# Performance work log

Measured on AMD Instinct MI355X. Metric: run time of the kernel, lower is better.

Reference implementation:

```python
import jax, jax.numpy as jnp
import numpy as np

N, D_IN, D, C, TOPK = 8192, 1024, 512, 2, 6
SCALE = D ** -0.5
LN_EPS = 1e-5


def setup_inputs() -> dict:
    key = jax.random.key(0)
    ks = jax.random.split(key, 20)
    s = 0.02
    p = {
        'x': jax.random.normal(ks[0], (N, D_IN), jnp.float32),
        'fc1_w': jax.random.normal(ks[1], (D_IN, D)) * s,
        'fc1_b': jnp.zeros((D,)),
        'wh_w': jax.random.normal(ks[2], (D, D)) * s,
        'wh_b': jnp.zeros((D,)),
        'wt_w': jax.random.normal(ks[3], (D, D)) * s,
        'wt_b': jnp.zeros((D,)),
        'lin1_w': jax.random.normal(ks[4], (D, D)) * s,
        'lin1_b': jnp.zeros((D,)),
        'lin2_w': jax.random.normal(ks[5], (D, D)) * s,
        'lin2_b': jnp.zeros((D,)),
        'att1_w': jax.random.normal(ks[6], (D, D // 2)) * s,
        'att1_b': jnp.zeros((D // 2,)),
        'att2_w': jax.random.normal(ks[7], (D // 2, 1)) * s,
        'att2_b': jnp.zeros((1,)),
        'ln_g': jnp.ones((D,)),
        'ln_b': jnp.zeros((D,)),
        'fc_w': jax.random.normal(ks[8], (D, C)) * s,
        'fc_b': jnp.zeros((C,)),
    }
    return p


def reference(x, fc1_w, fc1_b, wh_w, wh_b, wt_w, wt_b, lin1_w, lin1_b,
              lin2_w, lin2_b, att1_w, att1_b, att2_w, att2_b, ln_g, ln_b,
              fc_w, fc_b):
    # _fc1: Linear + ReLU (dropout = eval identity)
    h = jax.nn.relu(x @ fc1_w + fc1_b)                      # [N, D]
    h = (h + h.mean(axis=0, keepdims=True)) * 0.5
    e_h = h @ wh_w + wh_b                                   # [N, D]
    e_t = h @ wt_w + wt_b                                   # [N, D]
    # dense N x N attention logits, then top-k neighbors
    logits = (e_h * SCALE) @ e_t.T                          # [N, N]
    tw, ti = jax.lax.top_k(logits, TOPK)                    # [N, K]
    Nb_h = e_t[ti]                                          # [N, K, D] gather
    p = jax.nn.softmax(tw, axis=-1)                         # [N, K]
    # eh_r = p * Nb_h + (1 - p) * e_h  (the matmul in torch is a broadcast)
    eh_r = p[..., None] * Nb_h + (1.0 - p)[..., None] * e_h[:, None, :]
    gate = jnp.tanh(e_h[:, None, :] + eh_r)                 # [N, K, D]
    ka = jnp.einsum('nkd,nkd->nk', Nb_h, gate)              # [N, K]
    kp = jax.nn.softmax(ka, axis=-1)                        # [N, K]
    e_Nh = jnp.einsum('nk,nkd->nd', kp, Nb_h)               # [N, D]
    sum_e = jax.nn.leaky_relu((e_h + e_Nh) @ lin1_w + lin1_b)
    bi_e = jax.nn.leaky_relu((e_h * e_Nh) @ lin2_w + lin2_b)
    emb = sum_e + bi_e                                      # [N, D]
    # GlobalAttention readout over all N nodes (batch=None -> one graph)
    att = jax.nn.leaky_relu(emb @ att1_w + att1_b) @ att2_w + att2_b  # [N,1]
    a = jax.nn.softmax(att, axis=0)                         # [N, 1]
    pooled = jnp.sum(a * emb, axis=0, keepdims=True)        # [1, D]
    # LayerNorm
    mu = pooled.mean(axis=-1, keepdims=True)
    var = pooled.var(axis=-1, keepdims=True)
    ln = (pooled - mu) * jax.lax.rsqrt(var + LN_EPS) * ln_g + ln_b
    out = ln @ fc_w + fc_b                                  # [1, C]
    Y_prob = jax.nn.softmax(out, axis=-1)
    Y_hat = jnp.argmax(out, axis=-1, keepdims=True)
    return out, Y_prob, Y_hat
```

## Files before the change

### kernel.cpp

```cpp
#include <hip/hip_runtime.h>
#include <hip/hip_bf16.h>
#include <cstdint>
#include <math.h>

typedef unsigned short u16;
typedef unsigned int u32;
typedef __bf16 bh;
typedef bh bh8 __attribute__((ext_vector_type(8)));
typedef float f32x4 __attribute__((ext_vector_type(4)));

#define SCALE_F 0.04419417382415922f

__device__ __forceinline__ float bf2f(u16 u) {
    union { float f; unsigned int i; } v; v.i = ((unsigned int)u) << 16; return v.f;
}
__device__ __forceinline__ u16 f2bf(float f) {
    __hip_bfloat16 h = __float2bfloat16(f);
    return __builtin_bit_cast(u16, h);
}
__device__ __forceinline__ bh8 ld8_f32(const float* p) {
    float4 f0 = *(const float4*)p;
    float4 f1 = *(const float4*)(p + 4);
    bh8 r;
    r[0] = (bh)f0.x; r[1] = (bh)f0.y; r[2] = (bh)f0.z; r[3] = (bh)f0.w;
    r[4] = (bh)f1.x; r[5] = (bh)f1.y; r[6] = (bh)f1.z; r[7] = (bh)f1.w;
    return r;
}

__device__ __forceinline__ u32 ordf(float f) {
    u32 u = __float_as_uint(f);
    return u ^ ((u32)((int)u >> 31) | 0x80000000u);
}
__device__ __forceinline__ float unordf(u32 s) {
    u32 u = (s & 0x80000000u) ? (s ^ 0x80000000u) : ~s;
    return __uint_as_float(u);
}
__device__ __forceinline__ u32 pack_vi(float v, int inv_idx) {
    return (ordf(v) & 0xFFFFFF00u) | (u32)inv_idx;
}
__device__ __forceinline__ float unpack_v(u32 p) {
    return unordf(p & 0xFFFFFF00u);
}

__device__ __forceinline__ void gl_lds16(const u16* g, u16* l) {
    __builtin_amdgcn_global_load_lds(
        (const __attribute__((address_space(1))) void*)g,
        (__attribute__((address_space(3))) void*)l, 16, 0, 0);
}

__device__ __forceinline__ void xcd_swz(int bid, int& x, int& y) {
    int xcd = bid & 7, idx = bid >> 3;
    x = idx >> 3;
    y = xcd * 8 + (idx & 7);
}

__global__ void transpose_cvt(const float* s0, u16* d0, const float* s1, u16* d1,
                              const float* s2, u16* d2, const float* s3, u16* d3,
                              const float* s4, u16* d4, const float* s5, u16* d5,
                              const float* xs, u16* xd) {
    int b = blockIdx.x;
    if (b >= 1664) {
        int t = threadIdx.y * 32 + threadIdx.x;
        size_t i = ((size_t)(b - 1664) * 256 + t) * 8;
        *(bh8*)(xd + i) = ld8_f32(xs + i);
        return;
    }
    __shared__ float tsh[32][33];
    const float* src; u16* dst; int R, C, tt;
    if      (b < 512)  { src = s0; dst = d0; R = 1024; C = 512; tt = b; }
    else if (b < 768)  { src = s1; dst = d1; R = 512;  C = 512; tt = b - 512; }
    else if (b < 1024) { src = s2; dst = d2; R = 512;  C = 512; tt = b - 768; }
    else if (b < 1280) { src = s3; dst = d3; R = 512;  C = 512; tt = b - 1024; }
    else if (b < 1536) { src = s4; dst = d4; R = 512;  C = 512; tt = b - 1280; }
    else               { src = s5; dst = d5; R = 512;  C = 256; tt = b - 1536; }
    int ntx = C >> 5;
    int bx = (tt % ntx) * 32, by = (tt / ntx) * 32;
    int x = threadIdx.x, y = threadIdx.y;
    for (int i = 0; i < 32; i += 8)
        tsh[y + i][x] = src[(size_t)(by + y + i) * C + bx + x];
    __syncthreads();
    for (int i = 0; i < 32; i += 8)
        dst[(size_t)(bx + y + i) * R + by + x] = f2bf(tsh[x][y + i]);
}

template<int KT, int NF>
__device__ __forceinline__ void kloop64(const u16* __restrict__ Ag, const u16* __restrict__ Bg,
                                        u16* Alds, u16* Blds, f32x4 (&acc)[2][NF]) {
    const int tid = threadIdx.x;
    const int wave = tid >> 6, lane = tid & 63;
    const int lr = lane & 15, quad = lane >> 4;
    const int wm = (wave & 1) * 32, wn = (wave >> 1) * (NF * 16);
    const int r = tid >> 2;
    const int g8 = (((tid & 3) ^ ((tid >> 3) & 3))) * 8;
    const int kbr8 = (quad ^ ((lr >> 1) & 3)) * 8;
    const u16* ga  = Ag + (size_t)r * KT + g8;
    const u16* gb0 = Bg + (size_t)r * KT + g8;
    const u16* gb1 = gb0 + (size_t)64 * KT;
    u16* la = Alds + wave * 512;
    u16* lb = Blds + wave * 512;
    #pragma unroll
    for (int k0 = 0; k0 < KT; k0 += 32) {
        __syncthreads();
        gl_lds16(ga + k0, la);
        gl_lds16(gb0 + k0, lb);
        if (NF == 4) gl_lds16(gb1 + k0, lb + 2048);
        __syncthreads();
        bh8 af[2], bf_[NF];
        #pragma unroll
        for (int i = 0; i < 2; i++)
            af[i] = *(const bh8*)&Alds[(wm + i * 16 + lr) * 32 + kbr8];
        #pragma unroll
        for (int i = 0; i < NF; i++)
            bf_[i] = *(const bh8*)&Blds[(wn + i * 16 + lr) * 32 + kbr8];
        #pragma unroll
        for (int mi = 0; mi < 2; mi++)
            #pragma unroll
            for (int ni = 0; ni < NF; ni++)
                acc[mi][ni] = __builtin_amdgcn_mfma_f32_16x16x32_bf16(
                    af[mi], bf_[ni], acc[mi][ni], 0, 0, 0);
    }
}

template<int ACT, int F32OUT>
__device__ __forceinline__ void epilogue64(f32x4 (&acc)[2][2], const float* bias,
                                           float* Cf, u16* Cb, int N, int m0, int n0) {
    const int tid = threadIdx.x;
    const int wave = tid >> 6, lane = tid & 63;
    const int lr = lane & 15, quad = lane >> 4;
    const int wm = (wave & 1) * 32, wn = (wave >> 1) * 32;
    #pragma unroll
    for (int ni = 0; ni < 2; ni++) {
        int col = n0 + wn + ni * 16 + lr;
        float bs = bias[col];
        #pragma unroll
        for (int mi = 0; mi < 2; mi++) {
            #pragma unroll
            for (int i = 0; i < 4; i++) {
                int row = m0 + wm + mi * 16 + quad * 4 + i;
                float v = acc[mi][ni][i] + bs;
                if (ACT == 1) v = fmaxf(v, 0.0f);
                if (ACT == 2) v = (v > 0.0f) ? v : 0.01f * v;
                size_t o = (size_t)row * N + col;
                if (F32OUT) Cf[o] = v;
                else        Cb[o] = f2bf(v);
            }
        }
    }
}

template<int ACT, int F32OUT, int KT>
__global__ __launch_bounds__(256) void gemm64(
    const u16* __restrict__ A, const u16* __restrict__ B, const float* __restrict__ bias,
    float* __restrict__ Cf, u16* __restrict__ Cb, int N)
{
    __shared__ __align__(16) u16 Alds[64 * 32];
    __shared__ __align__(16) u16 Blds[64 * 32];
    const int m0 = blockIdx.y * 64, n0 = blockIdx.x * 64;
    f32x4 acc[2][2] = {};
    kloop64<KT, 2>(A + (size_t)m0 * KT, B + (size_t)n0 * KT, Alds, Blds, acc);
    epilogue64<ACT, F32OUT>(acc, bias, Cf, Cb, N, m0, n0);
}

template<int KT>
__device__ __forceinline__ void kloop128p(const u16* __restrict__ Ag,
                                          const u16* __restrict__ Bg,
                                          u16* lds, f32x4 (&acc)[4][4]) {
    const int tid = threadIdx.x;
    const int wave = tid >> 6, lane = tid & 63;
    const int lr = lane & 15, quad = lane >> 4;
    const int wm = (wave & 1) * 64, wn = (wave >> 1) * 64;
    const int r = tid >> 2;
    const int g8 = (((tid & 3) ^ ((tid >> 3) & 3))) * 8;
    const int kbr8 = (quad ^ ((lr >> 1) & 3)) * 8;
    const u16* ga0 = Ag + (size_t)r * KT + g8;
    const u16* ga1 = ga0 + (size_t)64 * KT;
    const u16* gb0 = Bg + (size_t)r * KT + g8;
    const u16* gb1 = gb0 + (size_t)64 * KT;
    const int wofs = wave * 512;
    constexpr int NT = KT / 32;
    gl_lds16(ga0,      lds + wofs);
    gl_lds16(ga1,      lds + wofs + 2048);
    gl_lds16(gb0,      lds + 4096 + wofs);
    gl_lds16(gb1,      lds + 4096 + wofs + 2048);
    gl_lds16(ga0 + 32, lds + 8192 + wofs);
    gl_lds16(ga1 + 32, lds + 8192 + wofs + 2048);
    gl_lds16(gb0 + 32, lds + 8192 + 4096 + wofs);
    gl_lds16(gb1 + 32, lds + 8192 + 4096 + wofs + 2048);
    #pragma unroll
    for (int t = 0; t < NT; t++) {
        if (t + 1 < NT) asm volatile("s_waitcnt vmcnt(4)" ::: "memory");
        else            asm volatile("s_waitcnt vmcnt(0)" ::: "memory");
        __builtin_amdgcn_s_barrier();
        if (t + 2 < NT) {
            const int k2 = (t + 2) * 32;
            u16* b = lds + ((t + 2) % 3) * 8192;
            gl_lds16(ga0 + k2, b + wofs);
            gl_lds16(ga1 + k2, b + wofs + 2048);
            gl_lds16(gb0 + k2, b + 4096 + wofs);
            gl_lds16(gb1 + k2, b + 4096 + wofs + 2048);
        }
        const u16* Ab = lds + (t % 3) * 8192;
        const u16* Bb = Ab + 4096;
        bh8 af[4], bf_[4];
        #pragma unroll
        for (int i = 0; i < 4; i++) {
            af[i]  = *(const bh8*)&Ab[(wm + i * 16 + lr) * 32 + kbr8];
            bf_[i] = *(const bh8*)&Bb[(wn + i * 16 + lr) * 32 + kbr8];
        }
        __builtin_amdgcn_s_setprio(1);
        #pragma unroll
        for (int mi = 0; mi < 4; mi++)
            #pragma unroll
            for (int ni = 0; ni < 4; ni++)
                acc[mi][ni] = __builtin_amdgcn_mfma_f32_16x16x32_bf16(
                    af[mi], bf_[ni], acc[mi][ni], 0, 0, 0);
        __builtin_amdgcn_s_setprio(0);
    }
}

template<int ACT, int F32OUT>
__device__ __forceinline__ void epilogue128(f32x4 (&acc)[4][4], const float* bias,
                                            float* Cf, u16* Cb, int N, int m0, int n0) {
    const int tid = threadIdx.x;
    const int wave = tid >> 6, lane = tid & 63;
    const int lr = lane & 15, quad = lane >> 4;
    const int wm = (wave & 1) * 64, wn = (wave >> 1) * 64;
    #pragma unroll
    for (int ni = 0; ni < 4; ni++) {
        int col = n0 + wn + ni * 16 + lr;
        float bs = bias[col];
        #pragma unroll
        for (int mi = 0; mi < 4; mi++) {
            #pragma unroll
            for (int i = 0; i < 4; i++) {
                int row = m0 + wm + mi * 16 + quad * 4 + i;
                float v = acc[mi][ni][i] + bs;
                if (ACT == 1) v = fmaxf(v, 0.0f);
                if (ACT == 2) v = (v > 0.0f) ? v : 0.01f * v;
                size_t o = (size_t)row * N + col;
                if (F32OUT) Cf[o] = v;
                else        Cb[o] = f2bf(v);
            }
        }
    }
}

template<int ACT, int F32OUT, int KT, int GNX>
__global__ __launch_bounds__(256) void gemm128(
    const u16* __restrict__ A, const u16* __restrict__ B, const float* __restrict__ bias,
    float* __restrict__ Cf, u16* __restrict__ Cb, int N)
{
    __shared__ __align__(16) u16 ldsbuf[3 * 8192];
    int bx, by;
    xcd_swz(blockIdx.y * GNX + blockIdx.x, bx, by);
    const int m0 = by * 128, n0 = bx * 128;
    f32x4 acc[4][4] = {};
    kloop128p<KT>(A + (size_t)m0 * KT, B + (size_t)n0 * KT, ldsbuf, acc);
    epilogue128<ACT, F32OUT>(acc, bias, Cf, Cb, N, m0, n0);
}

__global__ __launch_bounds__(256) void ehet128(
    const u16* __restrict__ A, const u16* __restrict__ Bh, const u16* __restrict__ Bt,
    const float* __restrict__ bh_, const float* __restrict__ bt_,
    u16* __restrict__ Oh, u16* __restrict__ Ot)
{
    __shared__ __align__(16) u16 ldsbuf[3 * 8192];
    int bx, by;
    xcd_swz(blockIdx.y * 8 + blockIdx.x, bx, by);
    const int m0 = by * 128, n0 = (bx & 3) * 128;
    const u16* B = (bx < 4) ? Bh : Bt;
    const float* bias = (bx < 4) ? bh_ : bt_;
    u16* O = (bx < 4) ? Oh : Ot;
    f32x4 acc[4][4] = {};
    kloop128p<512>(A + (size_t)m0 * 512, B + (size_t)n0 * 512, ldsbuf, acc);
    epilogue128<0, 0>(acc, bias, nullptr, O, 512, m0, n0);
}

__global__ __launch_bounds__(256) void lin12_64(
    const u16* __restrict__ A1, const u16* __restrict__ B1, const float* __restrict__ b1,
    const u16* __restrict__ A2, const u16* __restrict__ B2, const float* __restrict__ b2,
    u16* __restrict__ O)
{
    __shared__ __align__(16) u16 Alds[64 * 32];
    __shared__ __align__(16) u16 Blds[64 * 32];
    const int m0 = blockIdx.y * 64, n0 = blockIdx.x * 64;
    f32x4 acc1[2][2] = {}, acc2[2][2] = {};
    kloop64<512, 2>(A1 + (size_t)m0 * 512, B1 + (size_t)n0 * 512, Alds, Blds, acc1);
    kloop64<512, 2>(A2 + (size_t)m0 * 512, B2 + (size_t)n0 * 512, Alds, Blds, acc2);
    const int tid = threadIdx.x;
    const int wave = tid >> 6, lane = tid & 63;
    const int lr = lane & 15, quad = lane >> 4;
    const int wm = (wave & 1) * 32, wn = (wave >> 1) * 32;
    #pragma unroll
    for (int ni = 0; ni < 2; ni++) {
        int col = n0 + wn + ni * 16 + lr;
        float bs1 = b1[col], bs2 = b2[col];
        #pragma unroll
        for (int mi = 0; mi < 2; mi++) {
            #pragma unroll
            for (int i = 0; i < 4; i++) {
                int row = m0 + wm + mi * 16 + quad * 4 + i;
                float v1 = acc1[mi][ni][i] + bs1;
                v1 = (v1 > 0.0f) ? v1 : 0.01f * v1;
                float v2 = acc2[mi][ni][i] + bs2;
                v2 = (v2 > 0.0f) ? v2 : 0.01f * v2;
                O[(size_t)row * 512 + col] = f2bf(v1 + v2);
            }
        }
    }
}

template<int KT>
__device__ __forceinline__ void kloop256w(const u16* __restrict__ Ag,
                                          const u16* __restrict__ Bg,
                                          u16* lds, f32x4 (&acc)[4][8]) {
    const int tid = threadIdx.x;
    const int wave = tid >> 6, lane = tid & 63;
    const int lr = lane & 15, quad = lane >> 4;
    const int wm = (wave & 1) * 64;
    const int r = tid >> 2;
    const int g8 = (((tid & 3) ^ ((tid >> 3) & 3))) * 8;
    const int kbr8 = (quad ^ ((lr >> 1) & 3)) * 8;
    const u16* ga0 = Ag + (size_t)r * KT + g8;
    const u16* ga1 = ga0 + (size_t)64 * KT;
    const u16* gb0 = Bg + (size_t)r * KT + g8;
    const u16* gb1 = gb0 + (size_t)64 * KT;
    const u16* gb2 = gb0 + (size_t)128 * KT;
    const u16* gb3 = gb0 + (size_t)192 * KT;
    const int wofs = wave * 512;
    constexpr int NT = KT / 32;
    constexpr int BUF = 12288;
    auto stage = [&](int t, int koff) {
        u16* b = lds + (t % 3) * BUF;
        gl_lds16(ga0 + koff, b + wofs);
        gl_lds16(ga1 + koff, b + wofs + 2048);
        gl_lds16(gb0 + koff, b + 4096 + wofs);
        gl_lds16(gb1 + koff, b + 4096 + wofs + 2048);
        gl_lds16(gb2 + koff, b + 8192 + wofs);
        gl_lds16(gb3 + koff, b + 8192 + wofs + 2048);
    };
    stage(0, 0);
    stage(1, 32);
    #pragma unroll
    for (int t = 0; t < NT; t++) {
        if (t + 1 < NT) asm volatile("s_waitcnt vmcnt(6)" ::: "memory");
        else            asm volatile("s_waitcnt vmcnt(0)" ::: "memory");
        __builtin_amdgcn_s_barrier();
        if (t + 2 < NT) stage(t + 2, (t + 2) * 32);
        const u16* Ab = lds + (t % 3) * BUF;
        const u16* Bb = Ab + 4096 + (wave >> 1) * 4096;
        bh8 af[4];
        #pragma unroll
        for (int i = 0; i < 4; i++)
            af[i] = *(const bh8*)&Ab[(wm + i * 16 + lr) * 32 + kbr8];
        __builtin_amdgcn_s_setprio(1);
        #pragma unroll
        for (int g = 0; g < 2; g++) {
            bh8 bf_[4];
            #pragma unroll
            for (int j = 0; j < 4; j++)
                bf_[j] = *(const bh8*)&Bb[((g * 4 + j) * 16 + lr) * 32 + kbr8];
            #pragma unroll
            for (int mi = 0; mi < 4; mi++)
                #pragma unroll
                for (int j = 0; j < 4; j++)
                    acc[mi][g * 4 + j] = __builtin_amdgcn_mfma_f32_16x16x32_bf16(
                        af[mi], bf_[j], acc[mi][g * 4 + j], 0, 0, 0);
        }
        __builtin_amdgcn_s_setprio(0);
    }
}

__global__ __launch_bounds__(256, 2) void logits_topk(
    const u16* __restrict__ Ah, const u16* __restrict__ Bt, u32* __restrict__ tvp)
{
    __shared__ __align__(16) u16 ldsbuf[3 * 12288];
    u32* S = (u32*)ldsbuf;
    const int tid = threadIdx.x;
    int bx, by;
    xcd_swz(blockIdx.y * 32 + blockIdx.x, bx, by);
    const int m0 = by * 128;
    const int cb0 = bx * 256;
    const int lane = tid & 63, wave = tid >> 6;
    const int wh = wave & 1;
    const int wnh = wave >> 1;
    const int lr = lane & 15, quad = lane >> 4;
    const int srow = tid >> 2, scg = tid & 3;

    f32x4 acc[4][8] = {};
    kloop256w<512>(Ah + (size_t)m0 * 512, Bt + (size_t)cb0 * 512, ldsbuf, acc);

    u32 v[2][6] = {{0,0,0,0,0,0},{0,0,0,0,0,0}};
    #pragma unroll
    for (int h = 0; h < 2; h++) {
        #pragma unroll
        for (int nh = 0; nh < 2; nh++) {
            __syncthreads();
            if (wh == h && wnh == nh) {
                #pragma unroll
                for (int mi = 0; mi < 4; mi++)
                    #pragma unroll
                    for (int f = 0; f < 8; f++)
                        #pragma unroll
                        for (int i = 0; i < 4; i++) {
                            int colLocal = nh * 128 + f * 16 + lr;
                            S[(mi * 16 + quad * 4 + i) * 129 + f * 16 + lr]
                                = pack_vi(acc[mi][f][i], 255 - colLocal);
                        }
            }
            __syncthreads();
            const u32* Sr = &S[srow * 129 + scg * 8];
            #pragma unroll
            for (int ch = 0; ch < 4; ch++) {
                #pragma unroll
                for (int c = 0; c < 8; c++) {
                    u32 x = Sr[ch * 32 + c];
                    v[h][5] = max(v[h][5], min(v[h][4], x));
                    v[h][4] = max(v[h][4], min(v[h][3], x));
                    v[h][3] = max(v[h][3], min(v[h][2], x));
                    v[h][2] = max(v[h][2], min(v[h][1], x));
                    v[h][1] = max(v[h][1], min(v[h][0], x));
                    v[h][0] = max(v[h][0], x);
                }
            }
        }
    }
    #pragma unroll
    for (int h = 0; h < 2; h++) {
        __syncthreads();
        {
            u32* dst = &S[srow * 129 + scg * 6];
            #pragma unroll
            for (int j = 0; j < 6; j++) dst[j] = v[h][j];
        }
        __syncthreads();
        if (tid < 64) {
            u32 m0v = 0, m1v = 0, m2v = 0, m3v = 0, m4v = 0, m5v = 0;
            const u32* Sr = &S[tid * 129];
            #pragma unroll
            for (int s = 0; s < 24; s++) {
                u32 x = Sr[s];
                m5v = max(m5v, min(m4v, x));
                m4v = max(m4v, min(m3v, x));
                m3v = max(m3v, min(m2v, x));
                m2v = max(m2v, min(m1v, x));
                m1v = max(m1v, min(m0v, x));
                m0v = max(m0v, x);
            }
            u32* dst = tvp + (size_t)(m0 + h * 64 + tid) * 192 + bx * 6;
            dst[0] = m0v; dst[1] = m1v; dst[2] = m2v;
            dst[3] = m3v; dst[4] = m4v; dst[5] = m5v;
        }
    }
}

__global__ void topk_merge(const u32* __restrict__ tvp,
                           float* __restrict__ tv, int* __restrict__ ti)
{
    int r = blockIdx.x * 64 + threadIdx.x;
    u32 v[6]; int ix[6];
    #pragma unroll
    for (int j = 0; j < 6; j++) { v[j] = 0; ix[j] = 0; }
    const u32* pv = tvp + (size_t)r * 192;
    for (int b = 0; b < 32; b++) {
        #pragma unroll
        for (int j2 = 0; j2 < 6; j2++) {
            u32 p = pv[b * 6 + j2];
            if (p <= v[5]) break;
            v[5] = p; ix[5] = b * 256 + 255 - (int)(p & 255u);
            #pragma unroll
            for (int j = 5; j > 0; j--) {
                if (v[j] > v[j - 1]) {
                    u32 tf = v[j]; v[j] = v[j - 1]; v[j - 1] = tf;
                    int tx = ix[j]; ix[j] = ix[j - 1]; ix[j - 1] = tx;
                }
            }
        }
    }
    #pragma unroll
    for (int j = 0; j < 6; j++) {
        tv[(size_t)r * 6 + j] = unpack_v(v[j]) * SCALE_F;
        ti[(size_t)r * 6 + j] = ix[j];
    }
}

__global__ __launch_bounds__(256) void neighbor_kernel(
    const u16* __restrict__ eH, const u16* __restrict__ eT,
    const float* __restrict__ tv, const int* __restrict__ ti,
    u16* __restrict__ s1, u16* __restrict__ s2)
{
    const int tid = threadIdx.x, wave = tid >> 6, lane = tid & 63;
    const int n = blockIdx.x * 4 + wave;
    float tw[6]; int id[6];
    #pragma unroll
    for (int j = 0; j < 6; j++) {
        tw[j] = tv[n * 6 + j];
        int t = ti[n * 6 + j];
        id[j] = ((unsigned)t < 8192u) ? t : 0;
    }
    float mx = tw[0];
    #pragma unroll
    for (int j = 1; j < 6; j++) mx = fmaxf(mx, tw[j]);
    float p[6]; float ps = 0.f;
    #pragma unroll
    for (int j = 0; j < 6; j++) { p[j] = __expf(tw[j] - mx); ps += p[j]; }
    float inv = 1.0f / ps;
    #pragma unroll
    for (int j = 0; j < 6; j++) p[j] *= inv;

    const size_t base = (size_t)n * 512 + lane * 8;
    float eh[8];
    { bh8 v = *(const bh8*)(eH + base);
      #pragma unroll
      for (int c = 0; c < 8; c++) eh[c] = (float)v[c]; }
    float nb[6][8];
    #pragma unroll
    for (int j = 0; j < 6; j++) {
        bh8 v = *(const bh8*)(eT + (size_t)id[j] * 512 + lane * 8);
        #pragma unroll
        for (int c = 0; c < 8; c++) nb[j][c] = (float)v[c];
    }
    float ka[6];
    #pragma unroll
    for (int j = 0; j < 6; j++) {
        float s = 0.f;
        #pragma unroll
        for (int c = 0; c < 8; c++) {
            float e = p[j] * nb[j][c] + (1.f - p[j]) * eh[c];
            float x = eh[c] + e;
            x = fminf(fmaxf(x, -15.f), 15.f);
            float ex = __expf(2.f * x);
            float g = 1.f - 2.f / (ex + 1.f);
            s += nb[j][c] * g;
        }
        #pragma unroll
        for (int off = 32; off > 0; off >>= 1) s += __shfl_down(s, off);
        ka[j] = __shfl(s, 0);
    }
    float m2 = ka[0];
    #pragma unroll
    for (int j = 1; j < 6; j++) m2 = fmaxf(m2, ka[j]);
    float kp[6]; float ks = 0.f;
    #pragma unroll
    for (int j = 0; j < 6; j++) { kp[j] = __expf(ka[j] - m2); ks += kp[j]; }
    float inv2 = 1.0f / ks;
    #pragma unroll
    for (int j = 0; j < 6; j++) kp[j] *= inv2;
    bh8 o1, o2;
    #pragma unroll
    for (int c = 0; c < 8; c++) {
        float eN = 0.f;
        #pragma unroll
        for (int j = 0; j < 6; j++) eN += kp[j] * nb[j][c];
        o1[c] = (bh)(eh[c] + eN);
        o2[c] = (bh)(eh[c] * eN);
    }
    *(bh8*)(s1 + base) = o1;
    *(bh8*)(s2 + base) = o2;
}

__global__ void colsum_kernel(const u16* __restrict__ h, float* __restrict__ colsum) {
    int tid = threadIdx.x;
    int n0 = blockIdx.x * 32;
    float a0 = 0.f, a1 = 0.f;
    for (int k = 0; k < 32; k++) {
        size_t b = (size_t)(n0 + k) * 512;
        a0 += bf2f(h[b + tid]); a1 += bf2f(h[b + tid + 256]);
    }
    atomicAdd(&colsum[tid], a0);
    atomicAdd(&colsum[tid + 256], a1);
}

__global__ void meanmix_kernel(u16* __restrict__ h, const float* __restrict__ colsum) {
    size_t i = ((size_t)blockIdx.x * 256 + threadIdx.x) * 8;
    int col = (int)(i & 511);
    union { int4 v; u16 s[8]; } u;
    u.v = *(const int4*)&h[i];
    #pragma unroll
    for (int j = 0; j < 8; j++)
        u.s[j] = f2bf((bf2f(u.s[j]) + colsum[col + j] * (1.0f / 8192.0f)) * 0.5f);
    *(int4*)&h[i] = u.v;
}

__global__ __launch_bounds__(256) void att2_kernel(
    const float* __restrict__ a1, const float* __restrict__ w,
    const float* __restrict__ b, float* __restrict__ att)
{
    int row = blockIdx.x * 4 + (threadIdx.x >> 6);
    int lane = threadIdx.x & 63;
    const float* pr = a1 + (size_t)row * 256;
    float s = 0.f;
    #pragma unroll
    for (int k = 0; k < 4; k++) { int c = lane + k * 64; s += pr[c] * w[c]; }
    #pragma unroll
    for (int off = 32; off > 0; off >>= 1) s += __shfl_down(s, off);
    if (lane == 0) att[row] = s + b[0];
}

__global__ void att_max(const float* __restrict__ att, u32* __restrict__ scal_u) {
    int i = blockIdx.x * 256 + threadIdx.x;
    int lane = threadIdx.x & 63;
    u32 o = ordf(att[i]);
    #pragma unroll
    for (int off = 32; off > 0; off >>= 1) o = max(o, (u32)__shfl_down((int)o, off));
    if (lane == 0) atomicMax(&scal_u[0], o);
}
__global__ void att_sum(const float* __restrict__ att, float* __restrict__ scal) {
    int i = blockIdx.x * 256 + threadIdx.x;
    int lane = threadIdx.x & 63;
    float mx = unordf(((const u32*)scal)[0]);
    float e = __expf(att[i] - mx);
    #pragma unroll
    for (int off = 32; off > 0; off >>= 1) e += __shfl_down(e, off);
    if (lane == 0) atomicAdd(&scal[1], e);
}

__global__ void pooled_kernel(const u16* __restrict__ emb, const float* __restrict__ att,
                              const float* __restrict__ scal, float* __restrict__ pooled) {
    int tid = threadIdx.x;
    int n0 = blockIdx.x * 32;
    float mx = unordf(((const u32*)scal)[0]);
    float inv = 1.0f / scal[1];
    float a0 = 0.f, a1 = 0.f;
    for (int k = 0; k < 32; k++) {
        int n = n0 + k;
        float w = __expf(att[n] - mx) * inv;
        size_t b = (size_t)n * 512;
        a0 += w * bf2f(emb[b + tid]);
        a1 += w * bf2f(emb[b + tid + 256]);
    }
    atomicAdd(&pooled[tid], a0);
    atomicAdd(&pooled[tid + 256], a1);
}

__global__ void final_kernel(const float* __restrict__ pooled,
                             const float* __restrict__ g, const float* __restrict__ bln,
                             const float* __restrict__ fcw, const float* __restrict__ fcb,
                             float* __restrict__ out) {
    __shared__ float red[256];
    int tid = threadIdx.x;
    float x0 = pooled[tid], x1 = pooled[tid + 256];
    red[tid] = x0 + x1; __syncthreads();
    for (int s = 128; s > 0; s >>= 1) { if (tid < s) red[tid] += red[tid + s]; __syncthreads(); }
    float mu = red[0] * (1.0f / 512.0f); __syncthreads();
    float d0 = x0 - mu, d1 = x1 - mu;
    red[tid] = d0 * d0 + d1 * d1; __syncthreads();
    for (int s = 128; s > 0; s >>= 1) { if (tid < s) red[tid] += red[tid + s]; __syncthreads(); }
    float var = red[0] * (1.0f / 512.0f); __syncthreads();
    float rstd = rsqrtf(var + 1e-5f);
    float l0 = d0 * rstd * g[tid]       + bln[tid];
    float l1 = d1 * rstd * g[tid + 256] + bln[tid + 256];
    red[tid] = l0 * fcw[tid * 2] + l1 * fcw[(tid + 256) * 2]; __syncthreads();
    for (int s = 128; s > 0; s >>= 1) { if (tid < s) red[tid] += red[tid + s]; __syncthreads(); }
    float o0 = red[0] + fcb[0]; __syncthreads();
    red[tid] = l0 * fcw[tid * 2 + 1] + l1 * fcw[(tid + 256) * 2 + 1]; __syncthreads();
    for (int s = 128; s > 0; s >>= 1) { if (tid < s) red[tid] += red[tid + s]; __syncthreads(); }
    float o1 = red[0] + fcb[1];
    if (tid == 0) {
        float m = fmaxf(o0, o1);
        float e0 = expf(o0 - m), e1 = expf(o1 - m);
        float se = e0 + e1;
        out[0] = o0;
        out[1] = o1;
        out[2] = e0 / se;
        out[3] = e1 / se;
        out[4] = (o0 >= o1) ? 0.0f : 1.0f;
    }
}

extern "C" void kernel_launch(void* const* d_in, const int* in_sizes, int n_in,
                              void* d_out, int out_size, void* d_ws, size_t ws_size,
                              hipStream_t stream)
{
    const float* x      = (const float*)d_in[0];
    const float* fc1_w  = (const float*)d_in[1];
    const float* fc1_b  = (const float*)d_in[2];
    const float* wh_w   = (const float*)d_in[3];
    const float* wh_b   = (const float*)d_in[4];
    const float* wt_w   = (const float*)d_in[5];
    const float* wt_b   = (const float*)d_in[6];
    const float* lin1_w = (const float*)d_in[7];
    const float* lin1_b = (const float*)d_in[8];
    const float* lin2_w = (const float*)d_in[9];
    const float* lin2_b = (const float*)d_in[10];
    const float* att1_w = (const float*)d_in[11];
    const float* att1_b = (const float*)d_in[12];
    const float* att2_w = (const float*)d_in[13];
    const float* att2_b = (const float*)d_in[14];
    const float* ln_g   = (const float*)d_in[15];
    const float* ln_b   = (const float*)d_in[16];
    const float* fc_w   = (const float*)d_in[17];
    const float* fc_b   = (const float*)d_in[18];
    float* out = (float*)d_out;
    char* ws = (char*)d_ws;

    u16*   fc1T   = (u16*)(ws + 0);
    u16*   whT    = (u16*)(ws + 1048576);
    u16*   wtT    = (u16*)(ws + 1572864);
    u16*   l1T    = (u16*)(ws + 2097152);
    u16*   l2T    = (u16*)(ws + 2621440);
    u16*   a1T    = (u16*)(ws + 3145728);
    float* tv     = (float*)(ws + 3407872);
    int*   ti     = (int*)(ws + 3604480);
    float* att    = (float*)(ws + 3801088);
    float* colsum = (float*)(ws + 3833856);
    float* pooled = (float*)(ws + 3835904);
    float* scal   = (float*)(ws + 3837952);
    u32*   tvp    = (u32*)(ws + 4194304);
    u16*   hbf    = (u16*)(ws + 14680064);
    u16*   ehbf   = (u16*)(ws + 23068672);
    u16*   etbf   = (u16*)(ws + 31457280);
    u16*   s2bf   = (u16*)(ws + 39845888);
    u16*   xbf    = (u16*)(ws + 23068672);
    float* a1f    = (float*)(ws + 23068672);

    transpose_cvt<<<5760, dim3(32, 8), 0, stream>>>(
        fc1_w, fc1T, wh_w, whT, wt_w, wtT, lin1_w, l1T, lin2_w, l2T, att1_w, a1T, x, xbf);
    hipMemsetAsync(colsum, 0, 4160, stream);

    gemm128<1, 0, 1024, 4><<<dim3(4, 64), 256, 0, stream>>>(xbf, fc1T, fc1_b, nullptr, hbf, 512);
    colsum_kernel<<<256, 256, 0, stream>>>(hbf, colsum);
    meanmix_kernel<<<2048, 256, 0, stream>>>(hbf, colsum);

    ehet128<<<dim3(8, 64), 256, 0, stream>>>(hbf, whT, wtT, wh_b, wt_b, ehbf, etbf);

    logits_topk<<<dim3(32, 64), 256, 0, stream>>>(ehbf, etbf, tvp);
    topk_merge<<<128, 64, 0, stream>>>(tvp, tv, ti);

    neighbor_kernel<<<2048, 256, 0, stream>>>(ehbf, etbf, tv, ti, hbf, s2bf);

    lin12_64<<<dim3(8, 128), 256, 0, stream>>>(hbf, l1T, lin1_b, s2bf, l2T, lin2_b, etbf);

    gemm64<2, 1, 512><<<dim3(4, 128), 256, 0, stream>>>(etbf, a1T, att1_b, a1f, nullptr, 256);
    att2_kernel<<<2048, 256, 0, stream>>>(a1f, att2_w, att2_b, att);
    att_max<<<32, 256, 0, stream>>>(att, (u32*)scal);
    att_sum<<<32, 256, 0, stream>>>(att, scal);
    pooled_kernel<<<256, 256, 0, stream>>>(etbf, att, scal, pooled);

    final_kernel<<<1, 256, 0, stream>>>(pooled, ln_g, ln_b, fc_w, fc_b, out);
}
```

Baseline: 350.6 us.

## Pipeline 64-tile GEMM loads, register top-k via shuffles, bigger att1 tiles

Replaces the synchronous 64x64 k-loop with a triple-buffered global-to-LDS pipeline using vmcnt waits and setprio, used in lin12. The logits top-k epilogue now swaps MFMA operand order so each lane holds one row's column values, builds a per-lane top-6 in registers, merges across lanes with xor shuffles and across waves through a small LDS array. This removes the repeated LDS staging and barrier rounds. The att1 GEMM switches to the 128-tile kernel with fewer blocks. The change costs more register pressure and lowers occupancy in the att1 GEMM.

```diff
diff --git a/kernel.cpp b/kernel.cpp
--- a/kernel.cpp
+++ b/kernel.cpp
@@ -40,6 +40,15 @@
 }
 __device__ __forceinline__ float unpack_v(u32 p) {
     return unordf(p & 0xFFFFFF00u);
+}
+
+__device__ __forceinline__ void ins6(u32 (&v)[6], u32 x) {
+    v[5] = max(v[5], min(v[4], x));
+    v[4] = max(v[4], min(v[3], x));
+    v[3] = max(v[3], min(v[2], x));
+    v[2] = max(v[2], min(v[1], x));
+    v[1] = max(v[1], min(v[0], x));
+    v[0] = max(v[0], x);
 }
 
 __device__ __forceinline__ void gl_lds16(const u16* g, u16* l) {
@@ -83,82 +92,54 @@
         dst[(size_t)(bx + y + i) * R + by + x] = f2bf(tsh[x][y + i]);
 }
 
-template<int KT, int NF>
-__device__ __forceinline__ void kloop64(const u16* __restrict__ Ag, const u16* __restrict__ Bg,
-                                        u16* Alds, u16* Blds, f32x4 (&acc)[2][NF]) {
-    const int tid = threadIdx.x;
-    const int wave = tid >> 6, lane = tid & 63;
-    const int lr = lane & 15, quad = lane >> 4;
-    const int wm = (wave & 1) * 32, wn = (wave >> 1) * (NF * 16);
-    const int r = tid >> 2;
-    const int g8 = (((tid & 3) ^ ((tid >> 3) & 3))) * 8;
-    const int kbr8 = (quad ^ ((lr >> 1) & 3)) * 8;
-    const u16* ga  = Ag + (size_t)r * KT + g8;
-    const u16* gb0 = Bg + (size_t)r * KT + g8;
-    const u16* gb1 = gb0 + (size_t)64 * KT;
-    u16* la = Alds + wave * 512;
-    u16* lb = Blds + wave * 512;
-    #pragma unroll
-    for (int k0 = 0; k0 < KT; k0 += 32) {
-        __syncthreads();
-        gl_lds16(ga + k0, la);
-        gl_lds16(gb0 + k0, lb);
-        if (NF == 4) gl_lds16(gb1 + k0, lb + 2048);
-        __syncthreads();
-        bh8 af[2], bf_[NF];
-        #pragma unroll
-        for (int i = 0; i < 2; i++)
-            af[i] = *(const bh8*)&Alds[(wm + i * 16 + lr) * 32 + kbr8];
-        #pragma unroll
-        for (int i = 0; i < NF; i++)
-            bf_[i] = *(const bh8*)&Blds[(wn + i * 16 + lr) * 32 + kbr8];
-        #pragma unroll
-        for (int mi = 0; mi < 2; mi++)
-            #pragma unroll
-            for (int ni = 0; ni < NF; ni++)
-                acc[mi][ni] = __builtin_amdgcn_mfma_f32_16x16x32_bf16(
-                    af[mi], bf_[ni], acc[mi][ni], 0, 0, 0);
-    }
-}
-
-template<int ACT, int F32OUT>
-__device__ __forceinline__ void epilogue64(f32x4 (&acc)[2][2], const float* bias,
-                                           float* Cf, u16* Cb, int N, int m0, int n0) {
+template<int KT>
+__device__ __forceinline__ void kloop64p(const u16* __restrict__ Ag,
+                                         const u16* __restrict__ Bg,
+                                         u16* lds, f32x4 (&acc)[2][2]) {
     const int tid = threadIdx.x;
     const int wave = tid >> 6, lane = tid & 63;
     const int lr = lane & 15, quad = lane >> 4;
     const int wm = (wave & 1) * 32, wn = (wave >> 1) * 32;
-    #pragma unroll
-    for (int ni = 0; ni < 2; ni++) {
-        int col = n0 + wn + ni * 16 + lr;
-        float bs = bias[col];
-        #pragma unroll
-        for (int mi = 0; mi < 2; mi++) {
-            #pragma unroll
-            for (int i = 0; i < 4; i++) {
-                int row = m0 + wm + mi * 16 + quad * 4 + i;
-                float v = acc[mi][ni][i] + bs;
-                if (ACT == 1) v = fmaxf(v, 0.0f);
-                if (ACT == 2) v = (v > 0.0f) ? v : 0.01f * v;
-                size_t o = (size_t)row * N + col;
-                if (F32OUT) Cf[o] = v;
-                else        Cb[o] = f2bf(v);
-            }
-        }
-    }
-}
-
-template<int ACT, int F32OUT, int KT>
-__global__ __launch_bounds__(256) void gemm64(
-    const u16* __restrict__ A, const u16* __restrict__ B, const float* __restrict__ bias,
-    float* __restrict__ Cf, u16* __restrict__ Cb, int N)
-{
-    __shared__ __align__(16) u16 Alds[64 * 32];
-    __shared__ __align__(16) u16 Blds[64 * 32];
-    const int m0 = blockIdx.y * 64, n0 = blockIdx.x * 64;
-    f32x4 acc[2][2] = {};
-    kloop64<KT, 2>(A + (size_t)m0 * KT, B + (size_t)n0 * KT, Alds, Blds, acc);
-    epilogue64<ACT, F32OUT>(acc, bias, Cf, Cb, N, m0, n0);
+    const int r = tid >> 2;
+    const int g8 = (((tid & 3) ^ ((tid >> 3) & 3))) * 8;
+    const int kbr8 = (quad ^ ((lr >> 1) & 3)) * 8;
+    const u16* ga = Ag + (size_t)r * KT + g8;
+    const u16* gb = Bg + (size_t)r * KT + g8;
+    const int wofs = wave * 512;
+    constexpr int NT = KT / 32;
+    constexpr int BUF = 4096;
+    gl_lds16(ga,      lds + wofs);
+    gl_lds16(gb,      lds + 2048 + wofs);
+    gl_lds16(ga + 32, lds + BUF + wofs);
+    gl_lds16(gb + 32, lds + BUF + 2048 + wofs);
+    #pragma unroll
+    for (int t = 0; t < NT; t++) {
+        if (t + 1 < NT) asm volatile("s_waitcnt vmcnt(2)" ::: "memory");
+        else            asm volatile("s_waitcnt vmcnt(0)" ::: "memory");
+        __builtin_amdgcn_s_barrier();
+        if (t + 2 < NT) {
+            const int k2 = (t + 2) * 32;
+            u16* b = lds + ((t + 2) % 3) * BUF;
+            gl_lds16(ga + k2, b + wofs);
+            gl_lds16(gb + k2, b + 2048 + wofs);
+        }
+        const u16* Ab = lds + (t % 3) * BUF;
+        const u16* Bb = Ab + 2048;
+        bh8 af[2], bf_[2];
+        #pragma unroll
+        for (int i = 0; i < 2; i++) {
+            af[i]  = *(const bh8*)&Ab[(wm + i * 16 + lr) * 32 + kbr8];
+            bf_[i] = *(const bh8*)&Bb[(wn + i * 16 + lr) * 32 + kbr8];
+        }
+        __builtin_amdgcn_s_setprio(1);
+        #pragma unroll
+        for (int mi = 0; mi < 2; mi++)
+            #pragma unroll
+            for (int ni = 0; ni < 2; ni++)
+                acc[mi][ni] = __builtin_amdgcn_mfma_f32_16x16x32_bf16(
+                    af[mi], bf_[ni], acc[mi][ni], 0, 0, 0);
+        __builtin_amdgcn_s_setprio(0);
+    }
 }
 
 template<int KT>
@@ -281,12 +262,12 @@
     const u16* __restrict__ A2, const u16* __restrict__ B2, const float* __restrict__ b2,
     u16* __restrict__ O)
 {
-    __shared__ __align__(16) u16 Alds[64 * 32];
-    __shared__ __align__(16) u16 Blds[64 * 32];
+    __shared__ __align__(16) u16 ldsbuf[3 * 4096];
     const int m0 = blockIdx.y * 64, n0 = blockIdx.x * 64;
     f32x4 acc1[2][2] = {}, acc2[2][2] = {};
-    kloop64<512, 2>(A1 + (size_t)m0 * 512, B1 + (size_t)n0 * 512, Alds, Blds, acc1);
-    kloop64<512, 2>(A2 + (size_t)m0 * 512, B2 + (size_t)n0 * 512, Alds, Blds, acc2);
+    kloop64p<512>(A1 + (size_t)m0 * 512, B1 + (size_t)n0 * 512, ldsbuf, acc1);
+    __syncthreads();
+    kloop64p<512>(A2 + (size_t)m0 * 512, B2 + (size_t)n0 * 512, ldsbuf, acc2);
     const int tid = threadIdx.x;
     const int wave = tid >> 6, lane = tid & 63;
     const int lr = lane & 15, quad = lane >> 4;
@@ -316,10 +297,11 @@
                                           u16* lds, f32x4 (&acc)[4][8]) {
     const int tid = threadIdx.x;
     const int wave = tid >> 6, lane = tid & 63;
-    const int lr = lane & 15, quad = lane >> 4;
+    const int lr = lane & 15;
     const int wm = (wave & 1) * 64;
     const int r = tid >> 2;
     const int g8 = (((tid & 3) ^ ((tid >> 3) & 3))) * 8;
+    const int quad = lane >> 4;
     const int kbr8 = (quad ^ ((lr >> 1) & 3)) * 8;
     const u16* ga0 = Ag + (size_t)r * KT + g8;
     const u16* ga1 = ga0 + (size_t)64 * KT;
@@ -361,11 +343,11 @@
             for (int j = 0; j < 4; j++)
                 bf_[j] = *(const bh8*)&Bb[((g * 4 + j) * 16 + lr) * 32 + kbr8];
             #pragma unroll
-            for (int mi = 0; mi < 4; mi++)
+            for (int ai = 0; ai < 4; ai++)
                 #pragma unroll
                 for (int j = 0; j < 4; j++)
-                    acc[mi][g * 4 + j] = __builtin_amdgcn_mfma_f32_16x16x32_bf16(
-                        af[mi], bf_[j], acc[mi][g * 4 + j], 0, 0, 0);
+                    acc[ai][g * 4 + j] = __builtin_amdgcn_mfma_f32_16x16x32_bf16(
+                        bf_[j], af[ai], acc[ai][g * 4 + j], 0, 0, 0);
         }
         __builtin_amdgcn_s_setprio(0);
     }
@@ -375,81 +357,63 @@
     const u16* __restrict__ Ah, const u16* __restrict__ Bt, u32* __restrict__ tvp)
 {
     __shared__ __align__(16) u16 ldsbuf[3 * 12288];
-    u32* S = (u32*)ldsbuf;
+    __shared__ u32 Sx[128 * 6];
     const int tid = threadIdx.x;
     int bx, by;
     xcd_swz(blockIdx.y * 32 + blockIdx.x, bx, by);
     const int m0 = by * 128;
     const int cb0 = bx * 256;
     const int lane = tid & 63, wave = tid >> 6;
-    const int wh = wave & 1;
+    const int wm = (wave & 1) * 64;
     const int wnh = wave >> 1;
     const int lr = lane & 15, quad = lane >> 4;
-    const int srow = tid >> 2, scg = tid & 3;
 
     f32x4 acc[4][8] = {};
     kloop256w<512>(Ah + (size_t)m0 * 512, Bt + (size_t)cb0 * 512, ldsbuf, acc);
 
-    u32 v[2][6] = {{0,0,0,0,0,0},{0,0,0,0,0,0}};
-    #pragma unroll
-    for (int h = 0; h < 2; h++) {
-        #pragma unroll
-        for (int nh = 0; nh < 2; nh++) {
-            __syncthreads();
-            if (wh == h && wnh == nh) {
+    u32 L[4][6] = {{0,0,0,0,0,0},{0,0,0,0,0,0},{0,0,0,0,0,0},{0,0,0,0,0,0}};
+    #pragma unroll
+    for (int ai = 0; ai < 4; ai++)
+        #pragma unroll
+        for (int bi = 0; bi < 8; bi++)
+            #pragma unroll
+            for (int i = 0; i < 4; i++) {
+                int colLocal = wnh * 128 + bi * 16 + quad * 4 + i;
+                ins6(L[ai], pack_vi(acc[ai][bi][i], 255 - colLocal));
+            }
+    #pragma unroll
+    for (int m = 16; m <= 32; m <<= 1) {
+        #pragma unroll
+        for (int ai = 0; ai < 4; ai++) {
+            u32 o[6];
+            #pragma unroll
+            for (int j = 0; j < 6; j++)
+                o[j] = (u32)__shfl_xor((int)L[ai][j], m, 64);
+            #pragma unroll
+            for (int j = 0; j < 6; j++) ins6(L[ai], o[j]);
+        }
+    }
+    if (wnh == 1 && quad == 0) {
+        #pragma unroll
+        for (int ai = 0; ai < 4; ai++) {
+            u32* d = &Sx[(wm + ai * 16 + lr) * 6];
+            #pragma unroll
+            for (int j = 0; j < 6; j++) d[j] = L[ai][j];
+        }
+    }
+    __syncthreads();
+    if (wnh == 0) {
+        #pragma unroll
+        for (int ai = 0; ai < 4; ai++) {
+            const u32* p = &Sx[(wm + ai * 16 + lr) * 6];
+            #pragma unroll
+            for (int j = 0; j < 6; j++) ins6(L[ai], p[j]);
+            if (quad == 0) {
+                int row = m0 + wm + ai * 16 + lr;
+                u32* dst = tvp + (size_t)row * 192 + bx * 6;
                 #pragma unroll
-                for (int mi = 0; mi < 4; mi++)
-                    #pragma unroll
-                    for (int f = 0; f < 8; f++)
-                        #pragma unroll
-                        for (int i = 0; i < 4; i++) {
-                            int colLocal = nh * 128 + f * 16 + lr;
-                            S[(mi * 16 + quad * 4 + i) * 129 + f * 16 + lr]
-                                = pack_vi(acc[mi][f][i], 255 - colLocal);
-                        }
+                for (int j = 0; j < 6; j++) dst[j] = L[ai][j];
             }
-            __syncthreads();
-            const u32* Sr = &S[srow * 129 + scg * 8];
-            #pragma unroll
-            for (int ch = 0; ch < 4; ch++) {
-                #pragma unroll
-                for (int c = 0; c < 8; c++) {
-                    u32 x = Sr[ch * 32 + c];
-                    v[h][5] = max(v[h][5], min(v[h][4], x));
-                    v[h][4] = max(v[h][4], min(v[h][3], x));
-                    v[h][3] = max(v[h][3], min(v[h][2], x));
-                    v[h][2] = max(v[h][2], min(v[h][1], x));
-                    v[h][1] = max(v[h][1], min(v[h][0], x));
-                    v[h][0] = max(v[h][0], x);
-                }
-            }
-        }
-    }
-    #pragma unroll
-    for (int h = 0; h < 2; h++) {
-        __syncthreads();
-        {
-            u32* dst = &S[srow * 129 + scg * 6];
-            #pragma unroll
-            for (int j = 0; j < 6; j++) dst[j] = v[h][j];
-        }
-        __syncthreads();
-        if (tid < 64) {
-            u32 m0v = 0, m1v = 0, m2v = 0, m3v = 0, m4v = 0, m5v = 0;
-            const u32* Sr = &S[tid * 129];
-            #pragma unroll
-            for (int s = 0; s < 24; s++) {
-                u32 x = Sr[s];
-                m5v = max(m5v, min(m4v, x));
-                m4v = max(m4v, min(m3v, x));
-                m3v = max(m3v, min(m2v, x));
-                m2v = max(m2v, min(m1v, x));
-                m1v = max(m1v, min(m0v, x));
-                m0v = max(m0v, x);
-            }
-            u32* dst = tvp + (size_t)(m0 + h * 64 + tid) * 192 + bx * 6;
-            dst[0] = m0v; dst[1] = m1v; dst[2] = m2v;
-            dst[3] = m3v; dst[4] = m4v; dst[5] = m5v;
         }
     }
 }
@@ -731,7 +695,7 @@
 
     lin12_64<<<dim3(8, 128), 256, 0, stream>>>(hbf, l1T, lin1_b, s2bf, l2T, lin2_b, etbf);
 
-    gemm64<2, 1, 512><<<dim3(4, 128), 256, 0, stream>>>(etbf, a1T, att1_b, a1f, nullptr, 256);
+    gemm128<2, 1, 512, 2><<<dim3(2, 64), 256, 0, stream>>>(etbf, a1T, att1_b, a1f, nullptr, 256);
     att2_kernel<<<2048, 256, 0, stream>>>(a1f, att2_w, att2_b, att);
     att_max<<<32, 256, 0, stream>>>(att, (u32*)scal);
     att_sum<<<32, 256, 0, stream>>>(att, scal);
```

Result: slower. 372.5 us (+6.3%).
